# Kernel optimization log

Measured on AMD Instinct MI355X. Metric: run time of the kernel, lower is better.

## Reference

```python
import jax, jax.numpy as jnp
import numpy as np

N, H, DK, DV, DFF, D = 2, 8, 32, 32, 512, 256
B, S = 2, 2048
MASK_VALUE = -1e-30
EPS = 1e-14  # K.epsilon()**2 with default epsilon 1e-7


def glorot(key, shape):
    fan_in, fan_out = shape[-2], shape[-1]
    limit = np.sqrt(6.0 / (fan_in + fan_out))
    return jax.random.uniform(key, shape, jnp.float32, -limit, limit)


def setup_inputs() -> dict:
    key = jax.random.key(0)
    ks = jax.random.split(key, 8)
    return {
        "x": jax.random.normal(ks[0], (B, S, D), jnp.float32),
        "mask": jnp.ones((B, S), jnp.float32),
        "Wq": glorot(ks[1], (N, H, D, DK)),
        "Wk": glorot(ks[2], (N, H, D, DK)),
        "Wv": glorot(ks[3], (N, H, D, DV)),
        "Wo": glorot(ks[4], (N, H * DV, D)),
        "W1": glorot(ks[5], (N, D, DFF)),
        "b1": jnp.zeros((N, DFF), jnp.float32),
        "W2": glorot(ks[6], (N, DFF, D)),
        "b2": jnp.zeros((N, D), jnp.float32),
        "gamma": jnp.ones((2 * N,), jnp.float32),
        "beta": jnp.zeros((2 * N,), jnp.float32),
    }


def _layernorm(x, g, b):
    mean = jnp.mean(x, axis=-1, keepdims=True)
    var = jnp.mean(jnp.square(x - mean), axis=-1, keepdims=True)
    return (x - mean) / jnp.sqrt(var + EPS) * g + b


def reference(x, mask, Wq, Wk, Wv, Wo, W1, b1, W2, b2, gamma, beta):
    m = mask[:, None, None, :]  # [B,1,1,S], multiplies score rows' key axis
    for i in range(N):
        # batched multi-head attention (no 1/sqrt(dk) scaling, faithful to source)
        q = jnp.einsum("bsd,hdk->bhsk", x, Wq[i])
        k = jnp.einsum("bsd,hdk->bhsk", x, Wk[i])
        v = jnp.einsum("bsd,hdv->bhsv", x, Wv[i])
        A = jnp.einsum("bhsk,bhtk->bhst", q, k)  # [B,H,S,S]
        A = m * A + (1.0 - m) * MASK_VALUE
        A = jax.nn.softmax(A, axis=-1)
        o = jnp.einsum("bhst,bhtv->bhsv", A, v)
        conc = o.transpose(0, 2, 1, 3).reshape(x.shape[0], x.shape[1], H * DV)
        x = x + conc @ Wo[i]
        x = _layernorm(x, gamma[2 * i], beta[2 * i])
        ffn = jax.nn.relu(x @ W1[i] + b1[i]) @ W2[i] + b2[i]
        x = x + ffn
        x = _layernorm(x, gamma[2 * i + 1], beta[2 * i + 1])
    return x
```

## Files before the change

kernel.cpp:

```cpp
#include <hip/hip_runtime.h>
#include <hip/hip_bf16.h>

#define NL 2
#define NH 8
#define DKk 32
#define DVv 32
#define DFF 512
#define DD 256
#define BB 2
#define SS 2048
#define MROWS (BB*SS)
#define LN_EPS 1e-14f
#define L2E 1.4426950408889634f
#define SOFT_SHIFT_L2E (50.0f*L2E)

typedef __hip_bfloat16 bf16;
typedef unsigned short us;
typedef short bf16x8 __attribute__((ext_vector_type(8)));
typedef float f32x4  __attribute__((ext_vector_type(4)));
typedef unsigned short us4 __attribute__((ext_vector_type(4)));

#define O_XF   256
#define O_QB   (O_XF+1048576)
#define O_KH   (O_QB+1048576)
#define O_KL   (O_KH+524288)
#define O_VT   (O_KL+524288)
#define O_XH   (O_VT+524288)
#define O_XL   (O_XH+524288)
#define O_OP   (O_XL+524288)
#define O_ML   (O_OP+2097152)
#define O_MASK (O_ML+65536)
#define O_B1   (O_MASK+4096)
#define O_B2   (O_B1+1024)
#define O_GM   (O_B2+512)
#define O_BT   (O_GM+4)
#define O_PREP (O_BT+4)
#define TAIL_TOTAL (4096+1024+512+4+4)
#define CONV_BLOCKS (512 + (TAIL_TOTAL+255)/256)
#define PREP_BLOCKS 512
#define PQH 0u
#define PQL 393216u
#define POH 786432u
#define POL 917504u
#define P1H 1048576u
#define P1L 1310720u
#define P2H 1572864u
#define P2L 1835008u

__device__ __forceinline__ float us2f(us u){
  unsigned int v = ((unsigned int)u) << 16; float f;
  __builtin_memcpy(&f, &v, 4); return f;
}
__device__ __forceinline__ us f2bf_rne(float f){
  unsigned int b = __float_as_uint(f);
  b += 0x7FFFu + ((b>>16)&1u);
  return (us)(b>>16);
}

#if __has_builtin(__builtin_amdgcn_exp2f)
#define EXP2F(x) __builtin_amdgcn_exp2f(x)
#else
#define EXP2F(x) exp2f(x)
#endif

#if __has_builtin(__builtin_amdgcn_cvt_pk_bf16_f32)
typedef __bf16 bf16x2_t __attribute__((ext_vector_type(2)));
__device__ __forceinline__ int pack_bf16(float a, float b){
  bf16x2_t r = __builtin_amdgcn_cvt_pk_bf16_f32(a, b);
  int i; __builtin_memcpy(&i, &r, 4); return i;
}
#else
__device__ __forceinline__ int pack_bf16(float a, float b){
  int b0 = __float_as_int(a) + 0x8000;
  int b1 = __float_as_int(b) + 0x8000;
  return (b1 & 0xFFFF0000) | ((int)((unsigned)b0 >> 16));
}
#endif

__device__ __forceinline__ void gl_lds16(const us* g, us* l){
  __builtin_amdgcn_global_load_lds(
    (const __attribute__((address_space(1))) unsigned int*)g,
    (__attribute__((address_space(3))) unsigned int*)l, 16, 0, 0);
}

__device__ __forceinline__ size_t xhl_idx(int row, int col){
  int rt = row>>6, rg = (row>>4)&3, L15 = row&15;
  int kc = col>>5, Q = (col>>3)&3, j = col&7;
  return ((size_t)(rt*8+kc))*2048 + rg*512 + Q*128 + L15*8 + j;
}

__device__ __forceinline__ float conv1(const void* src, size_t i, int flag){
  if(flag) return ((const float*)src)[i];
  return us2f(((const us*)src)[i]);
}

__device__ __forceinline__ void prep_b_raw(const void* W0, const void* W1v, const void* W2v,
                                           int baseoff, us* __restrict__ Bh, us* __restrict__ Bl,
                                           int Kd, int Nd, int qkv, int g, int flag)
{
  int total = (Kd/32)*(Nd/16)*64;
  if(g >= total) return;
  int lane = g & 63, fi = g >> 6;
  int ncN = Nd/16;
  int nc = fi % ncN, kc = fi / ncN;
  int Q = lane>>4, L15 = lane&15;
  int n = nc*16 + L15;
  const void* src;
  int off0, stride;
  if(qkv){
    int sec = n>>8, h = (n>>5)&7, kq = n&31;
    src = (sec==0)?W0:((sec==1)?W1v:W2v);
    off0 = baseoff + h*8192 + kq;
    stride = 32;
  } else {
    src = W0;
    off0 = baseoff + n;
    stride = Nd;
  }
  #pragma unroll
  for(int j=0;j<8;j++){
    int k = kc*32 + Q*8 + j;
    float v = conv1(src, (size_t)off0 + (size_t)k*stride, flag);
    us hb = f2bf_rne(v);
    Bh[(size_t)g*8 + j] = hb;
    Bl[(size_t)g*8 + j] = f2bf_rne(v - us2f(hb));
  }
}

__global__ void conv_prep(const void* s0, const void* s1, const void* sWq, const void* sWk,
                          const void* sWv, const void* sWo, const void* sW1, const void* sb1,
                          const void* sW2, const void* sb2, const void* sgm, const void* sbt,
                          float* __restrict__ ws, int* __restrict__ flagp)
{
  __shared__ int fsh[4];
  int bad = 0;
  const us* xr = (const us*)s0;
  for(int i=threadIdx.x; i<4096; i+=256){
    float f = us2f(xr[i]);
    if(!(fabsf(f) < 1e3f)) bad = 1;
  }
  unsigned long long m = __ballot(bad);
  if((threadIdx.x&63)==0) fsh[threadIdx.x>>6] = (m!=0ull);
  __syncthreads();
  int flag = (fsh[0]|fsh[1]|fsh[2]|fsh[3]);
  if(blockIdx.x==0 && threadIdx.x==0) *flagp = flag;

  int b = blockIdx.x;
  if(b < PREP_BLOCKS){
    int layer = b >> 8, lb = b & 255;
    us* prep = (us*)(ws + O_PREP);
    if(lb < 96){
      int g = lb*256 + threadIdx.x;
      prep_b_raw(sWq, sWk, sWv, layer*65536, prep+PQH+(size_t)layer*196608,
                 prep+PQL+(size_t)layer*196608, 256, 768, 1, g, flag);
    } else if(lb < 128){
      int g = (lb-96)*256 + threadIdx.x;
      prep_b_raw(sWo, nullptr, nullptr, layer*65536, prep+POH+(size_t)layer*65536,
                 prep+POL+(size_t)layer*65536, 256, 256, 0, g, flag);
    } else if(lb < 192){
      int g = (lb-128)*256 + threadIdx.x;
      prep_b_raw(sW1, nullptr, nullptr, layer*131072, prep+P1H+(size_t)layer*131072,
                 prep+P1L+(size_t)layer*131072, 256, 512, 0, g, flag);
    } else {
      int g = (lb-192)*256 + threadIdx.x;
      prep_b_raw(sW2, nullptr, nullptr, layer*131072, prep+P2H+(size_t)layer*131072,
                 prep+P2L+(size_t)layer*131072, 512, 256, 0, g, flag);
    }
    return;
  }
  int b2 = b - PREP_BLOCKS;
  if(b2 < 512){
    int g8 = b2*256 + threadIdx.x;
    int e0 = g8*8;
    float v[8];
    if(flag){
      float4 a0 = *((const float4*)s0 + (e0>>2));
      float4 a1 = *((const float4*)s0 + (e0>>2) + 1);
      v[0]=a0.x; v[1]=a0.y; v[2]=a0.z; v[3]=a0.w;
      v[4]=a1.x; v[5]=a1.y; v[6]=a1.z; v[7]=a1.w;
    } else {
      bf16x8 u = *((const bf16x8*)s0 + g8);
      #pragma unroll
      for(int j=0;j<8;j++) v[j] = us2f((us)u[j]);
    }
    *(float4*)&ws[O_XF+e0]   = (float4){v[0],v[1],v[2],v[3]};
    *(float4*)&ws[O_XF+e0+4] = (float4){v[4],v[5],v[6],v[7]};
    union{ us a[8]; uint4 q; } hh, ll;
    #pragma unroll
    for(int j=0;j<8;j++){
      us hb = f2bf_rne(v[j]);
      hh.a[j] = hb;
      ll.a[j] = f2bf_rne(v[j] - us2f(hb));
    }
    size_t xi = xhl_idx(e0>>8, e0&255);
    *(uint4*)&((us*)(ws+O_XH))[xi] = hh.q;
    *(uint4*)&((us*)(ws+O_XL))[xi] = ll.q;
    return;
  }
  int g = (b2-512)*256 + threadIdx.x;
  if(g < 4096){ ws[O_MASK+g] = conv1(s1, g, flag)*L2E; return; }
  g -= 4096;
  if(g < 1024){ ws[O_B1+g] = conv1(sb1, g, flag); return; }
  g -= 1024;
  if(g < 512){ ws[O_B2+g] = conv1(sb2, g, flag); return; }
  g -= 512;
  if(g < 4){ ws[O_GM+g] = conv1(sgm, g, flag); return; }
  g -= 4;
  if(g < 4){ ws[O_BT+g] = conv1(sbt, g, flag); return; }
}

template<int MODE>
__launch_bounds__(256)
__global__ void gemm_mfma(const us* __restrict__ Axh, const us* __restrict__ Axl,
                          const us* __restrict__ Bh, const us* __restrict__ Bl,
                          const float* __restrict__ bias,
                          float* __restrict__ O,
                          us* __restrict__ QH, us* __restrict__ QL,
                          us* __restrict__ KH, us* __restrict__ KL, us* __restrict__ VT,
                          int Ncols, int Kdim)
{
  __shared__ __align__(16) us SH[16384];
  const int t = threadIdx.x;
  const int w = t>>6, lane = t&63;
  const int Q = lane>>4, L15 = lane&15;
  const int bx = blockIdx.x, by = blockIdx.y;
  const int row0 = bx*64;
  const int nc0 = by*4;
  const int col0 = by*64;
  const int nKc = Kdim>>5;
  const int ncW = Ncols>>4;

  f32x4 acc[2][2];
  #pragma unroll
  for(int i=0;i<2;i++)
    #pragma unroll
    for(int j=0;j<2;j++) acc[i][j] = (f32x4){0.f,0.f,0.f,0.f};

  auto stage = [&](int kc){
    const int bo = (kc&1)*8192;
    size_t abase = ((size_t)(bx*nKc + kc))*2048;
    gl_lds16(&Axh[abase + (size_t)t*8], &SH[bo + t*8]);
    gl_lds16(&Axl[abase + (size_t)t*8], &SH[bo + 2048 + t*8]);
    size_t gidx = ((size_t)(kc*ncW + nc0 + w)*64 + lane)*8;
    gl_lds16(&Bh[gidx], &SH[bo + 4096 + t*8]);
    gl_lds16(&Bl[gidx], &SH[bo + 6144 + t*8]);
  };

  stage(0);

  for(int kc=0; kc<nKc; kc++){
    __syncthreads();
    if(kc+1 < nKc) stage(kc+1);
    const int bo = (kc&1)*8192;
    const us* Ah  = SH + bo;
    const us* Al  = SH + bo + 2048;
    const us* Bhs = SH + bo + 4096;
    const us* Bls = SH + bo + 6144;

    bf16x8 aAh[2], aAl[2], bBh[2], bBl[2];
    #pragma unroll
    for(int rg2=0;rg2<2;rg2++){
      int rg = (w&1)*2 + rg2;
      aAh[rg2] = *(const bf16x8*)&Ah[rg*512 + lane*8];
      aAl[rg2] = *(const bf16x8*)&Al[rg*512 + lane*8];
    }
    #pragma unroll
    for(int cg2=0;cg2<2;cg2++){
      int nc = (w>>1)*2 + cg2;
      bBh[cg2] = *(const bf16x8*)&Bhs[nc*512 + lane*8];
      bBl[cg2] = *(const bf16x8*)&Bls[nc*512 + lane*8];
    }
    #pragma unroll
    for(int rg2=0;rg2<2;rg2++)
      #pragma unroll
      for(int cg2=0;cg2<2;cg2++){
        acc[rg2][cg2] = __builtin_amdgcn_mfma_f32_16x16x32_bf16(aAl[rg2], bBh[cg2], acc[rg2][cg2], 0,0,0);
        acc[rg2][cg2] = __builtin_amdgcn_mfma_f32_16x16x32_bf16(aAh[rg2], bBl[cg2], acc[rg2][cg2], 0,0,0);
        acc[rg2][cg2] = __builtin_amdgcn_mfma_f32_16x16x32_bf16(aAh[rg2], bBh[cg2], acc[rg2][cg2], 0,0,0);
      }
  }

  if(MODE==0){
    __syncthreads();
    us* TH = SH;
    us* TL = SH + 4608;
    #pragma unroll
    for(int rg2=0;rg2<2;rg2++)
      #pragma unroll
      for(int cg2=0;cg2<2;cg2++)
        #pragma unroll
        for(int r=0;r<4;r++){
          int rl = (w&1)*32 + rg2*16 + Q*4 + r;
          int cl = (w>>1)*32 + cg2*16 + L15;
          float va = acc[rg2][cg2][r];
          us hb = f2bf_rne(va);
          TH[rl*72+cl] = hb;
          TL[rl*72+cl] = f2bf_rne(va - us2f(hb));
        }
    __syncthreads();
    const int sec = col0>>8;
    const int h0  = (col0&255)>>5;
    const int b_  = row0>>11;
    const int srow0 = row0 & 2047;
    if(sec < 2){
      us* DH = (sec==0) ? QH : KH;
      us* DL = (sec==0) ? QL : KL;
      #pragma unroll
      for(int u2=0; u2<2; u2++){
        int u = w + u2*4;
        int rg = u&3, half = u>>2;
        int lbase = (rg*16 + L15)*72 + half*32 + Q*8;
        bf16x8 hv = *(const bf16x8*)&TH[lbase];
        bf16x8 lv = *(const bf16x8*)&TL[lbase];
        int bh = b_*NH + h0 + half;
        size_t dbase = ((size_t)(bh*128 + (srow0>>4) + rg)*64 + lane)*8;
        *(bf16x8*)&DH[dbase] = hv;
        *(bf16x8*)&DL[dbase] = lv;
      }
    } else {
      #pragma unroll
      for(int u2=0; u2<2; u2++){
        int u = w + u2*4;
        int sgrp = u&1, kqh = (u>>1)&1, half = u>>2;
        union{ us u8[8]; bf16x8 v; } vv;
        #pragma unroll
        for(int j=0;j<8;j++){
          int rl = sgrp*32 + Q*8 + j;
          int cl = half*32 + kqh*16 + L15;
          vv.u8[j] = TH[rl*72+cl];
        }
        int bh = b_*NH + h0 + half;
        size_t dbase = ((size_t)((bh*64 + (srow0>>5) + sgrp)*2 + kqh)*64 + lane)*8;
        *(bf16x8*)&VT[dbase] = vv.v;
      }
    }
  } else {
    #pragma unroll
    for(int rg2=0;rg2<2;rg2++)
      #pragma unroll
      for(int cg2=0;cg2<2;cg2++)
        #pragma unroll
        for(int r=0;r<4;r++){
          int row = row0 + (w&1)*32 + rg2*16 + Q*4 + r;
          int c   = col0 + (w>>1)*32 + cg2*16 + L15;
          float v = acc[rg2][cg2][r] + bias[c];
          O[(size_t)row*Ncols + c] = v>0.f ? v : 0.f;
        }
  }
}

__launch_bounds__(256)
__global__ void oln_ffn(const float* __restrict__ OpartA, const float* __restrict__ MLA,
                        const us* __restrict__ WOh, const us* __restrict__ WOl,
                        const us* __restrict__ W1h, const us* __restrict__ W1l,
                        const us* __restrict__ W2h, const us* __restrict__ W2l,
                        const float* __restrict__ b1, const float* __restrict__ b2,
                        float* __restrict__ xf, us* __restrict__ xh, us* __restrict__ xl,
                        const float* __restrict__ gamma, const float* __restrict__ beta, int gi0,
                        void* __restrict__ out, int write_out, const int* __restrict__ flagp)
{
  __shared__ __align__(16) us SH[32768];
  __shared__ __align__(16) us Ahs[1024], Als[1024];
  __shared__ __align__(16) us xAH[4096], xAL[4096];
  __shared__ __align__(16) us hAH[8192], hAL[8192];
  __shared__ float lred[128];
  const int t = threadIdx.x;
  const int w = t>>6, lane = t&63;
  const int Q = lane>>4, L15 = lane&15;
  const int row0 = blockIdx.x*16;

  auto stageW = [&](const us* Bh, const us* Bl, int fi0, int buf){
    const int bo = buf*16384;
    #pragma unroll
    for(int ii=0; ii<4; ii++){
      int u = w + ii*4;
      size_t gidx = ((size_t)(fi0 + u)*64 + lane)*8;
      gl_lds16(&Bh[gidx], &SH[bo + u*512 + lane*8]);
      gl_lds16(&Bl[gidx], &SH[bo + 8192 + u*512 + lane*8]);
    }
  };

  float4 pv0, pv1;
  float pl0 = 0.f, pl1 = 0.f;
  auto preloadA = [&](int kc){
    if(t < 128){
      int r = t>>3;
      int kl = (t&7)*4;
      int row = row0 + r;
      int b_ = row>>11, s_ = row&2047;
      size_t i0 = (size_t)(b_*8 + kc)*2048 + s_;
      pl0 = MLA[i0];
      pl1 = MLA[i0+32768];
      pv0 = *(const float4*)&OpartA[i0*32 + kl];
      pv1 = *(const float4*)&OpartA[(i0+32768)*32 + kl];
    }
  };
  auto writeA = [&](int kc){
    if(t < 128){
      int r = t>>3;
      int kl = (t&7)*4;
      float inv = 1.f/(pl0 + pl1);
      float f[4] = {(pv0.x+pv1.x)*inv, (pv0.y+pv1.y)*inv,
                    (pv0.z+pv1.z)*inv, (pv0.w+pv1.w)*inv};
      us4 h4, l4;
      #pragma unroll
      for(int j=0;j<4;j++){
        us hb = f2bf_rne(f[j]);
        h4[j] = hb; l4[j] = f2bf_rne(f[j] - us2f(hb));
      }
      int bo = (kc&1)*512;
      int off = (kl>>3)*128 + r*8 + (kl&7);
      *(us4*)&Ahs[bo+off] = h4;
      *(us4*)&Als[bo+off] = l4;
    }
  };

  f32x4 acc[4];
  #pragma unroll
  for(int cg=0;cg<4;cg++) acc[cg] = (f32x4){0.f,0.f,0.f,0.f};

  preloadA(0);
  stageW(WOh, WOl, 0, 0);
  writeA(0);

  for(int kc=0; kc<8; kc++){
    __syncthreads();
    if(kc < 7){
      preloadA(kc+1);
      stageW(WOh, WOl, (kc+1)*16, (kc+1)&1);
    } else {
      stageW(W1h, W1l, 0, 0);
    }
    const int bo = (kc&1)*16384;
    bf16x8 aAh = *(const bf16x8*)&Ahs[(kc&1)*512 + lane*8];
    bf16x8 aAl = *(const bf16x8*)&Als[(kc&1)*512 + lane*8];
    #pragma unroll
    for(int cg=0;cg<4;cg++){
      int u = w*4 + cg;
      bf16x8 bBh = *(const bf16x8*)&SH[bo + u*512 + lane*8];
      bf16x8 bBl = *(const bf16x8*)&SH[bo + 8192 + u*512 + lane*8];
      acc[cg] = __builtin_amdgcn_mfma_f32_16x16x32_bf16(aAl, bBh, acc[cg], 0,0,0);
      acc[cg] = __builtin_amdgcn_mfma_f32_16x16x32_bf16(aAh, bBl, acc[cg], 0,0,0);
      acc[cg] = __builtin_amdgcn_mfma_f32_16x16x32_bf16(aAh, bBh, acc[cg], 0,0,0);
    }
    if(kc < 7) writeA(kc+1);
  }

  float tmp[4][4];
  #pragma unroll
  for(int cg=0;cg<4;cg++)
    #pragma unroll
    for(int r=0;r<4;r++){
      int row = row0 + Q*4 + r;
      int c = w*64 + cg*16 + L15;
      tmp[cg][r] = acc[cg][r] + xf[(size_t)row*DD + c];
    }
  float s[4], sq[4];
  #pragma unroll
  for(int r=0;r<4;r++){
    s[r]  = tmp[0][r]+tmp[1][r]+tmp[2][r]+tmp[3][r];
    sq[r] = tmp[0][r]*tmp[0][r]+tmp[1][r]*tmp[1][r]+tmp[2][r]*tmp[2][r]+tmp[3][r]*tmp[3][r];
  }
  #pragma unroll
  for(int off=1; off<16; off<<=1)
    #pragma unroll
    for(int r=0;r<4;r++){
      s[r]  += __shfl_xor(s[r], off);
      sq[r] += __shfl_xor(sq[r], off);
    }
  if(L15==0){
    #pragma unroll
    for(int r=0;r<4;r++){
      int rl = Q*4 + r;
      lred[(w*16 + rl)*2]   = s[r];
      lred[(w*16 + rl)*2+1] = sq[r];
    }
  }
  __syncthreads();
  float val_s[4][4];
  {
    float g = gamma[gi0], bb = beta[gi0];
    float scv[4], mnv[4];
    #pragma unroll
    for(int r=0;r<4;r++){
      int rl = Q*4 + r;
      float S  = lred[rl*2]   + lred[(16+rl)*2]   + lred[(32+rl)*2]   + lred[(48+rl)*2];
      float SQ = lred[rl*2+1] + lred[(16+rl)*2+1] + lred[(32+rl)*2+1] + lred[(48+rl)*2+1];
      float mean = S*(1.f/DD);
      float var  = SQ*(1.f/DD) - mean*mean;
      scv[r] = rsqrtf(var+LN_EPS)*g;
      mnv[r] = mean;
    }
    #pragma unroll
    for(int cg=0;cg<4;cg++){
      int c = w*64 + cg*16 + L15;
      int base = (c>>5)*512 + (((c&31)>>3))*128 + (c&7);
      #pragma unroll
      for(int r=0;r<4;r++){
        float v = (tmp[cg][r]-mnv[r])*scv[r] + bb;
        val_s[cg][r] = v;
        us hb = f2bf_rne(v);
        xAH[base + (Q*4+r)*8] = hb;
        xAL[base + (Q*4+r)*8] = f2bf_rne(v - us2f(hb));
      }
    }
  }

  int step = 8;
  for(int nch=0; nch<2; nch++){
    f32x4 acc_h[4];
    #pragma unroll
    for(int cg=0;cg<4;cg++) acc_h[cg] = (f32x4){0.f,0.f,0.f,0.f};
    for(int kc=0; kc<8; kc++){
      __syncthreads();
      int ns = step - 8 + 1;
      if(ns < 16){
        stageW(W1h, W1l, (ns&7)*32 + (ns>>3)*16, (step+1)&1);
      } else {
        stageW(W2h, W2l, 0, (step+1)&1);
      }
      const int bo = (step&1)*16384;
      bf16x8 aAh = *(const bf16x8*)&xAH[kc*512 + lane*8];
      bf16x8 aAl = *(const bf16x8*)&xAL[kc*512 + lane*8];
      #pragma unroll
      for(int cg=0;cg<4;cg++){
        int u = w*4 + cg;
        bf16x8 bBh = *(const bf16x8*)&SH[bo + u*512 + lane*8];
        bf16x8 bBl = *(const bf16x8*)&SH[bo + 8192 + u*512 + lane*8];
        acc_h[cg] = __builtin_amdgcn_mfma_f32_16x16x32_bf16(aAl, bBh, acc_h[cg], 0,0,0);
        acc_h[cg] = __builtin_amdgcn_mfma_f32_16x16x32_bf16(aAh, bBl, acc_h[cg], 0,0,0);
        acc_h[cg] = __builtin_amdgcn_mfma_f32_16x16x32_bf16(aAh, bBh, acc_h[cg], 0,0,0);
      }
      step++;
    }
    #pragma unroll
    for(int cg=0;cg<4;cg++){
      int col = nch*256 + (w*4+cg)*16 + L15;
      float bv = b1[col];
      int base = (col>>5)*512 + (((col&31)>>3))*128 + (col&7);
      #pragma unroll
      for(int r=0;r<4;r++){
        int row = Q*4 + r;
        float v = acc_h[cg][r] + bv;
        v = v>0.f ? v : 0.f;
        us hb = f2bf_rne(v);
        hAH[base + row*8] = hb;
        hAL[base + row*8] = f2bf_rne(v - us2f(hb));
      }
    }
  }

  f32x4 acc_y[4];
  #pragma unroll
  for(int cg=0;cg<4;cg++) acc_y[cg] = (f32x4){0.f,0.f,0.f,0.f};
  for(int kc2=0; kc2<16; kc2++){
    __syncthreads();
    if(kc2+1 < 16) stageW(W2h, W2l, (kc2+1)*16, (step+1)&1);
    const int bo = (step&1)*16384;
    bf16x8 aAh = *(const bf16x8*)&hAH[kc2*512 + lane*8];
    bf16x8 aAl = *(const bf16x8*)&hAL[kc2*512 + lane*8];
    #pragma unroll
    for(int cg=0;cg<4;cg++){
      int u = w*4 + cg;
      bf16x8 bBh = *(const bf16x8*)&SH[bo + u*512 + lane*8];
      bf16x8 bBl = *(const bf16x8*)&SH[bo + 8192 + u*512 + lane*8];
      acc_y[cg] = __builtin_amdgcn_mfma_f32_16x16x32_bf16(aAl, bBh, acc_y[cg], 0,0,0);
      acc_y[cg] = __builtin_amdgcn_mfma_f32_16x16x32_bf16(aAh, bBl, acc_y[cg], 0,0,0);
      acc_y[cg] = __builtin_amdgcn_mfma_f32_16x16x32_bf16(aAh, bBh, acc_y[cg], 0,0,0);
    }
    step++;
  }

  float tmp2[4][4];
  #pragma unroll
  for(int cg=0;cg<4;cg++)
    #pragma unroll
    for(int r=0;r<4;r++){
      int c = w*64 + cg*16 + L15;
      tmp2[cg][r] = acc_y[cg][r] + val_s[cg][r] + b2[c];
    }
  float s2[4], sq2[4];
  #pragma unroll
  for(int r=0;r<4;r++){
    s2[r]  = tmp2[0][r]+tmp2[1][r]+tmp2[2][r]+tmp2[3][r];
    sq2[r] = tmp2[0][r]*tmp2[0][r]+tmp2[1][r]*tmp2[1][r]+tmp2[2][r]*tmp2[2][r]+tmp2[3][r]*tmp2[3][r];
  }
  #pragma unroll
  for(int off=1; off<16; off<<=1)
    #pragma unroll
    for(int r=0;r<4;r++){
      s2[r]  += __shfl_xor(s2[r], off);
      sq2[r] += __shfl_xor(sq2[r], off);
    }
  __syncthreads();
  if(L15==0){
    #pragma unroll
    for(int r=0;r<4;r++){
      int rl = Q*4 + r;
      lred[(w*16 + rl)*2]   = s2[r];
      lred[(w*16 + rl)*2+1] = sq2[r];
    }
  }
  __syncthreads();
  float g2 = gamma[gi0+1], bb2 = beta[gi0+1];
  float scv2[4], mnv2[4];
  #pragma unroll
  for(int r=0;r<4;r++){
    int rl = Q*4 + r;
    float S  = lred[rl*2]   + lred[(16+rl)*2]   + lred[(32+rl)*2]   + lred[(48+rl)*2];
    float SQ = lred[rl*2+1] + lred[(16+rl)*2+1] + lred[(32+rl)*2+1] + lred[(48+rl)*2+1];
    float mean = S*(1.f/DD);
    float var  = SQ*(1.f/DD) - mean*mean;
    scv2[r] = rsqrtf(var+LN_EPS)*g2;
    mnv2[r] = mean;
  }
  int flag = write_out ? *flagp : 0;
  #pragma unroll
  for(int cg=0;cg<4;cg++)
    #pragma unroll
    for(int r=0;r<4;r++){
      int row = row0 + Q*4 + r;
      int c = w*64 + cg*16 + L15;
      float val = (tmp2[cg][r]-mnv2[r])*scv2[r] + bb2;
      xf[(size_t)row*DD + c] = val;
      us hb = f2bf_rne(val);
      size_t xi = xhl_idx(row, c);
      xh[xi] = hb;
      xl[xi] = f2bf_rne(val - us2f(hb));
      if(write_out){
        if(flag) ((float*)out)[(size_t)row*DD + c] = val;
        else     ((bf16*)out)[(size_t)row*DD + c] = __float2bfloat16(val);
      }
    }
}

__launch_bounds__(256)
__global__ void attn_kernel(const us* __restrict__ QH, const us* __restrict__ QL,
                            const us* __restrict__ KH, const us* __restrict__ KL,
                            const us* __restrict__ VT,
                            const float* __restrict__ mask,
                            float* __restrict__ Opart, float* __restrict__ ML)
{
  __shared__ __align__(16) us Khs[4096], Kls[4096], Vts[4096];
  __shared__ __align__(16) float Msl[1024];
  const int t = threadIdx.x;
  const int bh = blockIdx.x >> 6;
  const int qt = (blockIdx.x & 63) >> 1;
  const int ks = blockIdx.x & 1;
  const int b_ = bh >> 3;
  const int wv = t >> 6;
  const int lane = t & 63;
  const int Q = lane >> 4, L15 = lane & 15;
  const int q0 = qt*64 + wv*16;

  size_t qidx = ((size_t)(bh*128 + qt*4 + wv)*64 + lane)*8;
  const bf16x8 qh_v = *(const bf16x8*)&QH[qidx];
  const bf16x8 ql_v = *(const bf16x8*)&QL[qidx];

  const us* KHbh = KH + (size_t)bh*65536;
  const us* KLbh = KL + (size_t)bh*65536;
  const us* VTbh = VT + (size_t)bh*65536;
  const int base = ks*1024;

  f32x4 Oa0a = {0.f,0.f,0.f,0.f}, Oa0b = {0.f,0.f,0.f,0.f};
  f32x4 Oa1a = {0.f,0.f,0.f,0.f}, Oa1b = {0.f,0.f,0.f,0.f};
  float lacc = 0.f;

  {
    const us* mrow = (const us*)(mask + (size_t)b_*SS + base);
    gl_lds16(mrow + (size_t)t*8, ((us*)Msl) + t*8);
    size_t kbase = (size_t)(base>>4)*512;
    size_t vbase = (size_t)(base>>5)*1024;
    gl_lds16(&KHbh[kbase + (size_t)t*8], &Khs[t*8]);
    gl_lds16(&KLbh[kbase + (size_t)t*8], &Kls[t*8]);
    gl_lds16(&VTbh[vbase + (size_t)t*8], &Vts[t*8]);
  }

  for(int s=0; s<16; s++){
    __syncthreads();
    if(s < 15){
      int t0n = base + (s+1)*64;
      int bn = (s+1)&1;
      size_t kbase = (size_t)(t0n>>4)*512;
      size_t vbase = (size_t)(t0n>>5)*1024;
      gl_lds16(&KHbh[kbase + (size_t)t*8], &Khs[bn*2048 + t*8]);
      gl_lds16(&KLbh[kbase + (size_t)t*8], &Kls[bn*2048 + t*8]);
      gl_lds16(&VTbh[vbase + (size_t)t*8], &Vts[bn*2048 + t*8]);
    }
    const int bo = (s&1)*2048;
    const int mo = s*64;

    f32x4 St[4];
    const f32x4 zz = {0.f,0.f,0.f,0.f};
    #pragma unroll
    for(int kt=0;kt<4;kt++){
      bf16x8 aKh = *(const bf16x8*)&Khs[bo + kt*512 + lane*8];
      bf16x8 aKl = *(const bf16x8*)&Kls[bo + kt*512 + lane*8];
      f32x4 a = __builtin_amdgcn_mfma_f32_16x16x32_bf16(aKl, qh_v, zz, 0,0,0);
      a = __builtin_amdgcn_mfma_f32_16x16x32_bf16(aKh, ql_v, a, 0,0,0);
      a = __builtin_amdgcn_mfma_f32_16x16x32_bf16(aKh, qh_v, a, 0,0,0);
      St[kt] = a;
    }

    float lsum = 0.f;
    #pragma unroll
    for(int kt=0;kt<4;kt++){
      float4 mv = *(const float4*)&Msl[mo + kt*16 + Q*4];
      float mvr[4] = {mv.x, mv.y, mv.z, mv.w};
      #pragma unroll
      for(int r=0;r<4;r++){
        float p = EXP2F(fmaf(mvr[r], St[kt][r], -SOFT_SHIFT_L2E));
        St[kt][r] = p;
        lsum += p;
      }
    }
    lacc += lsum;

    int pk[4][2];
    #pragma unroll
    for(int kt=0;kt<4;kt++){
      pk[kt][0] = pack_bf16(St[kt][0], St[kt][1]);
      pk[kt][1] = pack_bf16(St[kt][2], St[kt][3]);
    }

    #pragma unroll
    for(int c=0;c<2;c++){
      union { int i[4]; bf16x8 v; } bu;
      #pragma unroll
      for(int d=0;d<4;d++){
        int srcl = (((Q&1)*2 + (d>>1))<<4) | L15;
        int vlo = __shfl(pk[2*c  ][d&1], srcl, 64);
        int vhi = __shfl(pk[2*c+1][d&1], srcl, 64);
        bu.i[d] = (Q & 2) ? vhi : vlo;
      }
      bf16x8 aV0 = *(const bf16x8*)&Vts[bo + (c*2+0)*512 + lane*8];
      bf16x8 aV1 = *(const bf16x8*)&Vts[bo + (c*2+1)*512 + lane*8];
      if(c == 0){
        Oa0a = __builtin_amdgcn_mfma_f32_16x16x32_bf16(aV0, bu.v, Oa0a, 0,0,0);
        Oa1a = __builtin_amdgcn_mfma_f32_16x16x32_bf16(aV1, bu.v, Oa1a, 0,0,0);
      } else {
        Oa0b = __builtin_amdgcn_mfma_f32_16x16x32_bf16(aV0, bu.v, Oa0b, 0,0,0);
        Oa1b = __builtin_amdgcn_mfma_f32_16x16x32_bf16(aV1, bu.v, Oa1b, 0,0,0);
      }
    }
  }

  f32x4 Oa0 = Oa0a + Oa0b;
  f32x4 Oa1 = Oa1a + Oa1b;
  lacc += __shfl_xor(lacc, 16);
  lacc += __shfl_xor(lacc, 32);

  float* opp = &Opart[((size_t)(ks*16+bh)*SS + q0 + L15)*32];
  #pragma unroll
  for(int r=0;r<4;r++){
    opp[Q*4+r]    = Oa0[r];
    opp[16+Q*4+r] = Oa1[r];
  }
  if(Q==0){
    ML[(size_t)(ks*16+bh)*SS + q0 + L15] = lacc;
  }
}

extern "C" void kernel_launch(void* const* d_in, const int* in_sizes, int n_in,
                              void* d_out, int out_size, void* d_ws, size_t ws_size,
                              hipStream_t stream)
{
  float* ws = (float*)d_ws;
  int* flagp = (int*)d_ws;

  float* xf  = ws + O_XF;
  us* QHb = (us*)(ws + O_QB);
  us* QLb = QHb + 1048576;
  us* KH = (us*)(ws + O_KH);
  us* KL = (us*)(ws + O_KL);
  us* VT = (us*)(ws + O_VT);
  us* XH = (us*)(ws + O_XH);
  us* XL = (us*)(ws + O_XL);
  float* Opart = ws + O_OP;
  float* ML  = ws + O_ML;
  float* b1f = ws + O_B1;
  float* b2f_ = ws + O_B2;
  float* gmf = ws + O_GM;
  float* btf = ws + O_BT;
  us* prep = (us*)(ws + O_PREP);

  conv_prep<<<PREP_BLOCKS+CONV_BLOCKS,256,0,stream>>>(
      d_in[0], d_in[1], d_in[2], d_in[3], d_in[4], d_in[5],
      d_in[6], d_in[7], d_in[8], d_in[9], d_in[10], d_in[11],
      ws, flagp);

  for(int i=0;i<NL;i++){
    const float* b1i = b1f + (size_t)i*DFF;
    const float* b2i = b2f_ + (size_t)i*DD;

    dim3 g0(64, 12);
    gemm_mfma<0><<<g0,256,0,stream>>>(XH, XL,
                                      prep+PQH+(size_t)i*196608, prep+PQL+(size_t)i*196608,
                                      nullptr, nullptr,
                                      QHb, QLb, KH, KL, VT, 768, 256);
    attn_kernel<<<1024,256,0,stream>>>(QHb, QLb, KH, KL, VT, ws + O_MASK, Opart, ML);
    oln_ffn<<<256,256,0,stream>>>(Opart, ML,
                                  prep+POH+(size_t)i*65536, prep+POL+(size_t)i*65536,
                                  prep+P1H+(size_t)i*131072, prep+P1L+(size_t)i*131072,
                                  prep+P2H+(size_t)i*131072, prep+P2L+(size_t)i*131072,
                                  b1i, b2i, xf, XH, XL,
                                  gmf, btf, 2*i, d_out, (i==NL-1)?1:0, flagp);
  }
}
```

Before: 257.1 us.

## Load FFN/output-proj weight fragments directly from global instead of LDS staging

Removes the double-buffered LDS staging of Wo/W1/W2 fragments and the per-step block barriers, so each wave reads its pre-swizzled weight fragments straight from global memory (L2-resident) into registers. The attention-output A operand is also built per lane in registers rather than through shared memory. This cuts LDS footprint (possibly raising occupancy) and most barriers, at the cost of every wave issuing its own global loads with exposed latency, partly hidden by unroll-2.

```diff
diff --git a/kernel.cpp b/kernel.cpp
--- a/kernel.cpp
+++ b/kernel.cpp
@@ -359,8 +359,6 @@
                         const float* __restrict__ gamma, const float* __restrict__ beta, int gi0,
                         void* __restrict__ out, int write_out, const int* __restrict__ flagp)
 {
-  __shared__ __align__(16) us SH[32768];
-  __shared__ __align__(16) us Ahs[1024], Als[1024];
   __shared__ __align__(16) us xAH[4096], xAL[4096];
   __shared__ __align__(16) us hAH[8192], hAL[8192];
   __shared__ float lred[128];
@@ -368,82 +366,40 @@
   const int w = t>>6, lane = t&63;
   const int Q = lane>>4, L15 = lane&15;
   const int row0 = blockIdx.x*16;
-
-  auto stageW = [&](const us* Bh, const us* Bl, int fi0, int buf){
-    const int bo = buf*16384;
-    #pragma unroll
-    for(int ii=0; ii<4; ii++){
-      int u = w + ii*4;
-      size_t gidx = ((size_t)(fi0 + u)*64 + lane)*8;
-      gl_lds16(&Bh[gidx], &SH[bo + u*512 + lane*8]);
-      gl_lds16(&Bl[gidx], &SH[bo + 8192 + u*512 + lane*8]);
-    }
-  };
-
-  float4 pv0, pv1;
-  float pl0 = 0.f, pl1 = 0.f;
-  auto preloadA = [&](int kc){
-    if(t < 128){
-      int r = t>>3;
-      int kl = (t&7)*4;
-      int row = row0 + r;
-      int b_ = row>>11, s_ = row&2047;
-      size_t i0 = (size_t)(b_*8 + kc)*2048 + s_;
-      pl0 = MLA[i0];
-      pl1 = MLA[i0+32768];
-      pv0 = *(const float4*)&OpartA[i0*32 + kl];
-      pv1 = *(const float4*)&OpartA[(i0+32768)*32 + kl];
-    }
-  };
-  auto writeA = [&](int kc){
-    if(t < 128){
-      int r = t>>3;
-      int kl = (t&7)*4;
-      float inv = 1.f/(pl0 + pl1);
-      float f[4] = {(pv0.x+pv1.x)*inv, (pv0.y+pv1.y)*inv,
-                    (pv0.z+pv1.z)*inv, (pv0.w+pv1.w)*inv};
-      us4 h4, l4;
-      #pragma unroll
-      for(int j=0;j<4;j++){
-        us hb = f2bf_rne(f[j]);
-        h4[j] = hb; l4[j] = f2bf_rne(f[j] - us2f(hb));
-      }
-      int bo = (kc&1)*512;
-      int off = (kl>>3)*128 + r*8 + (kl&7);
-      *(us4*)&Ahs[bo+off] = h4;
-      *(us4*)&Als[bo+off] = l4;
-    }
-  };
+  const int b_ = row0>>11, s0_ = row0&2047;
 
   f32x4 acc[4];
   #pragma unroll
   for(int cg=0;cg<4;cg++) acc[cg] = (f32x4){0.f,0.f,0.f,0.f};
 
-  preloadA(0);
-  stageW(WOh, WOl, 0, 0);
-  writeA(0);
-
+  #pragma unroll 2
   for(int kc=0; kc<8; kc++){
-    __syncthreads();
-    if(kc < 7){
-      preloadA(kc+1);
-      stageW(WOh, WOl, (kc+1)*16, (kc+1)&1);
-    } else {
-      stageW(W1h, W1l, 0, 0);
-    }
-    const int bo = (kc&1)*16384;
-    bf16x8 aAh = *(const bf16x8*)&Ahs[(kc&1)*512 + lane*8];
-    bf16x8 aAl = *(const bf16x8*)&Als[(kc&1)*512 + lane*8];
+    size_t i0 = ((size_t)(b_*8 + kc))*2048 + s0_ + L15;
+    float l0 = MLA[i0], l1 = MLA[i0+32768];
+    float inv = 1.f/(l0 + l1);
+    const float* p0 = &OpartA[i0*32 + Q*8];
+    const float* p1 = &OpartA[(i0+32768)*32 + Q*8];
+    float4 a0 = *(const float4*)p0, a1 = *(const float4*)(p0+4);
+    float4 c0 = *(const float4*)p1, c1 = *(const float4*)(p1+4);
+    float fv[8];
+    fv[0]=(a0.x+c0.x)*inv; fv[1]=(a0.y+c0.y)*inv; fv[2]=(a0.z+c0.z)*inv; fv[3]=(a0.w+c0.w)*inv;
+    fv[4]=(a1.x+c1.x)*inv; fv[5]=(a1.y+c1.y)*inv; fv[6]=(a1.z+c1.z)*inv; fv[7]=(a1.w+c1.w)*inv;
+    union{ us a[8]; bf16x8 v; } Ahv, Alv;
+    #pragma unroll
+    for(int j=0;j<8;j++){
+      us hb = f2bf_rne(fv[j]);
+      Ahv.a[j] = hb;
+      Alv.a[j] = f2bf_rne(fv[j] - us2f(hb));
+    }
     #pragma unroll
     for(int cg=0;cg<4;cg++){
-      int u = w*4 + cg;
-      bf16x8 bBh = *(const bf16x8*)&SH[bo + u*512 + lane*8];
-      bf16x8 bBl = *(const bf16x8*)&SH[bo + 8192 + u*512 + lane*8];
-      acc[cg] = __builtin_amdgcn_mfma_f32_16x16x32_bf16(aAl, bBh, acc[cg], 0,0,0);
-      acc[cg] = __builtin_amdgcn_mfma_f32_16x16x32_bf16(aAh, bBl, acc[cg], 0,0,0);
-      acc[cg] = __builtin_amdgcn_mfma_f32_16x16x32_bf16(aAh, bBh, acc[cg], 0,0,0);
-    }
-    if(kc < 7) writeA(kc+1);
+      size_t fi = (size_t)(kc*16 + w*4 + cg)*512 + (size_t)lane*8;
+      bf16x8 bBh = *(const bf16x8*)&WOh[fi];
+      bf16x8 bBl = *(const bf16x8*)&WOl[fi];
+      acc[cg] = __builtin_amdgcn_mfma_f32_16x16x32_bf16(Alv.v, bBh, acc[cg], 0,0,0);
+      acc[cg] = __builtin_amdgcn_mfma_f32_16x16x32_bf16(Ahv.v, bBl, acc[cg], 0,0,0);
+      acc[cg] = __builtin_amdgcn_mfma_f32_16x16x32_bf16(Ahv.v, bBh, acc[cg], 0,0,0);
+    }
   }
 
   float tmp[4][4];
@@ -505,33 +461,26 @@
       }
     }
   }
-
-  int step = 8;
+  __syncthreads();
+
+  #pragma unroll
   for(int nch=0; nch<2; nch++){
     f32x4 acc_h[4];
     #pragma unroll
     for(int cg=0;cg<4;cg++) acc_h[cg] = (f32x4){0.f,0.f,0.f,0.f};
+    #pragma unroll 2
     for(int kc=0; kc<8; kc++){
-      __syncthreads();
-      int ns = step - 8 + 1;
-      if(ns < 16){
-        stageW(W1h, W1l, (ns&7)*32 + (ns>>3)*16, (step+1)&1);
-      } else {
-        stageW(W2h, W2l, 0, (step+1)&1);
-      }
-      const int bo = (step&1)*16384;
       bf16x8 aAh = *(const bf16x8*)&xAH[kc*512 + lane*8];
       bf16x8 aAl = *(const bf16x8*)&xAL[kc*512 + lane*8];
       #pragma unroll
       for(int cg=0;cg<4;cg++){
-        int u = w*4 + cg;
-        bf16x8 bBh = *(const bf16x8*)&SH[bo + u*512 + lane*8];
-        bf16x8 bBl = *(const bf16x8*)&SH[bo + 8192 + u*512 + lane*8];
+        size_t fi = (size_t)(kc*32 + nch*16 + w*4 + cg)*512 + (size_t)lane*8;
+        bf16x8 bBh = *(const bf16x8*)&W1h[fi];
+        bf16x8 bBl = *(const bf16x8*)&W1l[fi];
         acc_h[cg] = __builtin_amdgcn_mfma_f32_16x16x32_bf16(aAl, bBh, acc_h[cg], 0,0,0);
         acc_h[cg] = __builtin_amdgcn_mfma_f32_16x16x32_bf16(aAh, bBl, acc_h[cg], 0,0,0);
         acc_h[cg] = __builtin_amdgcn_mfma_f32_16x16x32_bf16(aAh, bBh, acc_h[cg], 0,0,0);
       }
-      step++;
     }
     #pragma unroll
     for(int cg=0;cg<4;cg++){
@@ -549,26 +498,24 @@
       }
     }
   }
+  __syncthreads();
 
   f32x4 acc_y[4];
   #pragma unroll
   for(int cg=0;cg<4;cg++) acc_y[cg] = (f32x4){0.f,0.f,0.f,0.f};
+  #pragma unroll 2
   for(int kc2=0; kc2<16; kc2++){
-    __syncthreads();
-    if(kc2+1 < 16) stageW(W2h, W2l, (kc2+1)*16, (step+1)&1);
-    const int bo = (step&1)*16384;
     bf16x8 aAh = *(const bf16x8*)&hAH[kc2*512 + lane*8];
     bf16x8 aAl = *(const bf16x8*)&hAL[kc2*512 + lane*8];
     #pragma unroll
     for(int cg=0;cg<4;cg++){
-      int u = w*4 + cg;
-      bf16x8 bBh = *(const bf16x8*)&SH[bo + u*512 + lane*8];
-      bf16x8 bBl = *(const bf16x8*)&SH[bo + 8192 + u*512 + lane*8];
+      size_t fi = (size_t)(kc2*16 + w*4 + cg)*512 + (size_t)lane*8;
+      bf16x8 bBh = *(const bf16x8*)&W2h[fi];
+      bf16x8 bBl = *(const bf16x8*)&W2l[fi];
       acc_y[cg] = __builtin_amdgcn_mfma_f32_16x16x32_bf16(aAl, bBh, acc_y[cg], 0,0,0);
       acc_y[cg] = __builtin_amdgcn_mfma_f32_16x16x32_bf16(aAh, bBl, acc_y[cg], 0,0,0);
       acc_y[cg] = __builtin_amdgcn_mfma_f32_16x16x32_bf16(aAh, bBh, acc_y[cg], 0,0,0);
     }
-    step++;
   }
 
   float tmp2[4][4];
```

Result: slower. 265.1 us (+3.1%).
